# Optimization experiments

Measured on AMD Instinct MI355X. Metric: run time of the kernel, lower is better.

## Reference

```python
import jax, jax.numpy as jnp
import numpy as np

N = 50000      # nodes
E = 800000     # edges
F_IN = 128     # input features
H = 8          # heads
F = 16         # features per head
NEG_SLOPE = 0.2


def setup_inputs() -> dict:
    key = jax.random.key(0)
    k_x, k_ei, k_w, k_as, k_ad = jax.random.split(key, 5)
    x = jax.random.normal(k_x, (N, F_IN), dtype=jnp.float32)
    edge_index = jax.random.randint(k_ei, (2, E), 0, N, dtype=jnp.int64)
    # learned params (PyG GATConv: lin weight [H*F, F_in] no bias; att_src/att_dst [H, F]; out bias [H*F])
    glorot = lambda k, shp: jax.random.uniform(k, shp, jnp.float32, -1.0, 1.0) * np.sqrt(6.0 / (shp[-1] + shp[-2]))
    W = glorot(k_w, (H * F, F_IN))
    att_src = glorot(k_as, (H, F))
    att_dst = glorot(k_ad, (H, F))
    bias = jnp.zeros((H * F,), dtype=jnp.float32)  # bias_init = zeros_
    return {"x": x, "W": W, "att_src": att_src, "att_dst": att_dst, "bias": bias, "edge_index": edge_index}


def reference(x, W, att_src, att_dst, bias, edge_index):
    # linear projection, split heads: [N, H, F]
    h = (x @ W.T).reshape(N, H, F)
    # per-node attention logits: [N, H]
    a_src = jnp.einsum('nhf,hf->nh', h, att_src)
    a_dst = jnp.einsum('nhf,hf->nh', h, att_dst)
    src, dst = edge_index[0], edge_index[1]
    # edge scores + LeakyReLU: [E, H]
    e = a_src[src] + a_dst[dst]
    e = jnp.where(e >= 0, e, NEG_SLOPE * e)
    # segment softmax over incoming edges of each dst node
    m = jax.ops.segment_max(e, dst, num_segments=N)          # [N, H]
    ex = jnp.exp(e - m[dst])                                  # [E, H]
    denom = jax.ops.segment_sum(ex, dst, num_segments=N)     # [N, H]
    alpha = ex / (denom[dst] + 1e-16)                         # [E, H]
    # weighted scatter-aggregate of source features
    msg = alpha[:, :, None] * h[src]                          # [E, H, F]
    out = jax.ops.segment_sum(msg, dst, num_segments=N)      # [N, H, F]
    return out.reshape(N, H * F) + bias
```

## Files before the change

kernel.cpp:

```cpp
#include <hip/hip_runtime.h>

#define NEG_SLOPE 0.2f
#define HEADS 8
#define FEAT 16
#define HF 128
#define FIN 128
#define BROWS 64
#define PITCH 136
#define BSHIFT 7
#define BNODES 128
#define MAXBUCK 512
#define EPT 16
#define SCAP 64
#define CAP 4096

typedef __bf16 bf16x8 __attribute__((ext_vector_type(8)));
typedef float  f32x4  __attribute__((ext_vector_type(4)));

__device__ __forceinline__ bool detect_i64(const int* ei) {
    return (ei[1] | ei[3] | ei[5] | ei[7]) == 0;
}
__device__ __forceinline__ int load_idx(const int* ei, long long pos, bool is64) {
    return is64 ? ei[2 * pos] : ei[pos];
}

__device__ __forceinline__ float bf2f(unsigned u) { return __uint_as_float(u << 16); }

__device__ __forceinline__ unsigned short f2bf(float f) {
    unsigned u = __float_as_uint(f);
    unsigned r = u + 0x7fffu + ((u >> 16) & 1u);
    return (unsigned short)(r >> 16);
}

__global__ __launch_bounds__(256) void proj_binsort_kernel(
    const float* __restrict__ x, const float* __restrict__ W,
    const float* __restrict__ att_src, const float* __restrict__ att_dst,
    unsigned short* __restrict__ hb, float* __restrict__ a_src,
    float* __restrict__ a_dst,
    const int* __restrict__ ei, unsigned* __restrict__ ebuf,
    int* __restrict__ cnt2, int N, int E, int nb, int nsb, int PB)
{
    __shared__ __align__(16) char smem[(BROWS + FIN) * PITCH * 2];
    const int t = threadIdx.x;

    if (blockIdx.x >= PB) {
        int* lh = (int*)smem;
        const int blk = blockIdx.x - PB;
        const bool is64 = detect_i64(ei);
        const int e0 = blk * (EPT * 256);

        for (int b = t; b < nb; b += 256) lh[b] = 0;
        __syncthreads();

#pragma unroll
        for (int i = 0; i < EPT; ++i) {
            const int e = e0 + i * 256 + t;
            if (e < E) {
                const unsigned s = (unsigned)load_idx(ei, e, is64);
                const unsigned d = (unsigned)load_idx(ei, (long long)E + e, is64);
                const unsigned pk = s | (d << 16);
                const int bkt = d >> BSHIFT;
                const int ofs = atomicAdd(&lh[bkt], 1);
                if (ofs < SCAP)
                    ebuf[((size_t)bkt * nsb + blk) * SCAP + ofs] = pk;
            }
        }
        __syncthreads();
        for (int b = t; b < nb; b += 256)
            cnt2[blk * MAXBUCK + b] = min(lh[b], SCAP);
        return;
    }

    unsigned short* xs  = (unsigned short*)smem;
    unsigned short* wsl = xs + BROWS * PITCH;
    const int n0 = blockIdx.x * BROWS;

#pragma unroll
    for (int i = 0; i < 8; ++i) {
        const int f4 = i * 256 + t;
        const int r = f4 >> 5, c4 = f4 & 31;
        const int rr = (n0 + r < N) ? (n0 + r) : (N - 1);
        const float4 v = ((const float4*)(x + (size_t)rr * FIN))[c4];
        unsigned short* p = &xs[r * PITCH + c4 * 4];
        p[0] = f2bf(v.x); p[1] = f2bf(v.y); p[2] = f2bf(v.z); p[3] = f2bf(v.w);
    }
#pragma unroll
    for (int i = 0; i < 16; ++i) {
        const int f4 = i * 256 + t;
        const int r = f4 >> 5, c4 = f4 & 31;
        const float4 v = ((const float4*)(W + (size_t)r * FIN))[c4];
        unsigned short* p = &wsl[r * PITCH + c4 * 4];
        p[0] = f2bf(v.x); p[1] = f2bf(v.y); p[2] = f2bf(v.z); p[3] = f2bf(v.w);
    }
    __syncthreads();

    const int w = t >> 6, lane = t & 63;
    const int lrow = lane & 15;
    const int lk = lane >> 4;
    const int r0 = w * 16;

    f32x4 acc[8];
#pragma unroll
    for (int i = 0; i < 8; ++i) { f32x4 z = {0.f, 0.f, 0.f, 0.f}; acc[i] = z; }

#pragma unroll
    for (int ks = 0; ks < 4; ++ks) {
        const int kb = ks * 32 + lk * 8;
        const bf16x8 af = *(const bf16x8*)&xs[(r0 + lrow) * PITCH + kb];
#pragma unroll
        for (int tt = 0; tt < 8; ++tt) {
            const bf16x8 bf = *(const bf16x8*)&wsl[(tt * 16 + lrow) * PITCH + kb];
            acc[tt] = __builtin_amdgcn_mfma_f32_16x16x32_bf16(af, bf, acc[tt], 0, 0, 0);
        }
    }
    __syncthreads();

#pragma unroll
    for (int tt = 0; tt < 8; ++tt) {
#pragma unroll
        for (int rg = 0; rg < 4; ++rg) {
            const int row = r0 + lk * 4 + rg;
            const int col = tt * 16 + lrow;
            xs[row * PITCH + col] = f2bf(acc[tt][rg]);
        }
    }
    __syncthreads();

#pragma unroll
    for (int i = 0; i < 8; ++i) {
        const int u4 = i * 256 + t;
        const int r = u4 >> 5, c4 = u4 & 31;
        if (n0 + r < N) {
            const unsigned short* p = &xs[r * PITCH + c4 * 4];
            ushort4 v; v.x = p[0]; v.y = p[1]; v.z = p[2]; v.w = p[3];
            ((ushort4*)hb)[(size_t)(n0 + r) * (HF / 4) + c4] = v;
        }
    }
#pragma unroll
    for (int i = 0; i < 2; ++i) {
        const int p = i * 256 + t;
        const int r = p >> 3, hd = p & 7;
        if (n0 + r < N) {
            float s = 0.f, d = 0.f;
#pragma unroll
            for (int j = 0; j < FEAT; ++j) {
                const float hv = bf2f(xs[r * PITCH + hd * FEAT + j]);
                s = fmaf(hv, att_src[hd * FEAT + j], s);
                d = fmaf(hv, att_dst[hd * FEAT + j], d);
            }
            a_src[(size_t)(n0 + r) * HEADS + hd] = s;
            a_dst[(size_t)(n0 + r) * HEADS + hd] = d;
        }
    }
}

__global__ __launch_bounds__(256) void bucket_csr(
    const unsigned* __restrict__ ebuf, const int* __restrict__ cnt2,
    int* __restrict__ row_start, int* __restrict__ csr_src,
    int* __restrict__ btot, int N, int nsb)
{
    __shared__ int scnt[256], soff[256];
    __shared__ unsigned ubuf[CAP];
    __shared__ int cnts[BNODES], sc[BNODES], cur[BNODES];
    const int b = blockIdx.x;
    const int t = threadIdx.x;

    const int v = (t < nsb) ? cnt2[t * MAXBUCK + b] : 0;
    scnt[t] = v;
    soff[t] = v;
    __syncthreads();
#pragma unroll
    for (int off = 1; off < 256; off <<= 1) {
        const int y = (t >= off) ? soff[t - off] : 0;
        __syncthreads();
        soff[t] += y;
        __syncthreads();
    }
    const int cntb = min(soff[255], CAP);
    const int myoff = soff[t] - v;
    __syncthreads();

    if (t < nsb && v > 0) {
        const unsigned* sp = ebuf + ((size_t)b * nsb + t) * SCAP;
        for (int j = 0; j < v; ++j) {
            const int o = myoff + j;
            if (o < CAP) ubuf[o] = sp[j];
        }
    }
    if (t < BNODES) cnts[t] = 0;
    __syncthreads();

    for (int j = t; j < cntb; j += 256)
        atomicAdd(&cnts[(ubuf[j] >> 16) & (BNODES - 1)], 1);
    __syncthreads();
    if (t < BNODES) sc[t] = cnts[t];
    __syncthreads();
#pragma unroll
    for (int off = 1; off < BNODES; off <<= 1) {
        const int y = (t < BNODES && t >= off) ? sc[t - off] : 0;
        __syncthreads();
        if (t < BNODES) sc[t] += y;
        __syncthreads();
    }
    if (t < BNODES) {
        const int excl = sc[t] - cnts[t];
        const int node = b * BNODES + t;
        if (node < N) row_start[node] = b * CAP + excl;
        cur[t] = excl;
    }
    if (t == 0) btot[b] = cntb;
    __syncthreads();
    for (int j = t; j < cntb; j += 256) {
        const unsigned p = ubuf[j];
        const int dl = (p >> 16) & (BNODES - 1);
        const int ofs = atomicAdd(&cur[dl], 1);
        csr_src[(size_t)b * CAP + ofs] = (int)(p & 0xffffu);
    }
}

__global__ __launch_bounds__(64) void agg_kernel(
    const int* __restrict__ csr_src, const int* __restrict__ row_start,
    const int* __restrict__ btot, const float* __restrict__ a_src,
    const float* __restrict__ a_dst, const unsigned short* __restrict__ hb,
    const float* __restrict__ bias, float* __restrict__ out, int N)
{
    const int d = blockIdx.x;
    const int t = threadIdx.x;
    const int hd = t >> 3;
    const int b = d >> BSHIFT, dl = d & (BNODES - 1);
    const int beg = row_start[d];
    const int end = (dl == BNODES - 1 || d == N - 1)
                  ? (b * CAP + btot[b]) : row_start[d + 1];
    const float adh = a_dst[d * HEADS + hd];

    float acc0 = 0.f, acc1 = 0.f, den = 0.f;
    for (int c = beg; c < end; c += 64) {
        const int m = min(64, end - c);
        const int sreg = (t < m) ? csr_src[c + t] : 0;
        int j = 0;
        for (; j + 8 <= m; j += 8) {
            int s[8]; unsigned p[8]; float w[8];
#pragma unroll
            for (int k = 0; k < 8; ++k) s[k] = __shfl(sreg, j + k, 64);
#pragma unroll
            for (int k = 0; k < 8; ++k)
                p[k] = *(const unsigned*)(hb + (size_t)s[k] * HF + 2 * t);
#pragma unroll
            for (int k = 0; k < 8; ++k) {
                float v = a_src[s[k] * HEADS + hd] + adh;
                v = v >= 0.f ? v : NEG_SLOPE * v;
                w[k] = __expf(v);
            }
#pragma unroll
            for (int k = 0; k < 8; ++k) {
                acc0 = fmaf(w[k], bf2f(p[k] & 0xffffu), acc0);
                acc1 = fmaf(w[k], bf2f(p[k] >> 16),     acc1);
                den += w[k];
            }
        }
        for (; j + 4 <= m; j += 4) {
            int s[4]; unsigned p[4]; float w[4];
#pragma unroll
            for (int k = 0; k < 4; ++k) s[k] = __shfl(sreg, j + k, 64);
#pragma unroll
            for (int k = 0; k < 4; ++k)
                p[k] = *(const unsigned*)(hb + (size_t)s[k] * HF + 2 * t);
#pragma unroll
            for (int k = 0; k < 4; ++k) {
                float v = a_src[s[k] * HEADS + hd] + adh;
                v = v >= 0.f ? v : NEG_SLOPE * v;
                w[k] = __expf(v);
            }
#pragma unroll
            for (int k = 0; k < 4; ++k) {
                acc0 = fmaf(w[k], bf2f(p[k] & 0xffffu), acc0);
                acc1 = fmaf(w[k], bf2f(p[k] >> 16),     acc1);
                den += w[k];
            }
        }
        for (; j < m; ++j) {
            const int s = __shfl(sreg, j, 64);
            const unsigned p = *(const unsigned*)(hb + (size_t)s * HF + 2 * t);
            float v = a_src[s * HEADS + hd] + adh;
            v = v >= 0.f ? v : NEG_SLOPE * v;
            const float w = __expf(v);
            acc0 = fmaf(w, bf2f(p & 0xffffu), acc0);
            acc1 = fmaf(w, bf2f(p >> 16), acc1);
            den += w;
        }
    }
    const float inv = 1.f / (den + 1e-16f);
    const float2 b2 = ((const float2*)bias)[t];
    float2 o2;
    o2.x = fmaf(acc0, inv, b2.x);
    o2.y = fmaf(acc1, inv, b2.y);
    ((float2*)out)[(size_t)d * (HF / 2) + t] = o2;
}

extern "C" void kernel_launch(void* const* d_in, const int* in_sizes, int n_in,
                              void* d_out, int out_size, void* d_ws, size_t ws_size,
                              hipStream_t stream)
{
    const float* x       = (const float*)d_in[0];
    const float* W       = (const float*)d_in[1];
    const float* att_src = (const float*)d_in[2];
    const float* att_dst = (const float*)d_in[3];
    const float* bias    = (const float*)d_in[4];
    const int*   ei      = (const int*)d_in[5];
    float* out = (float*)d_out;

    const int N = in_sizes[0] / FIN;
    const int E = in_sizes[5] / 2;
    const int NBUCK = (N + BNODES - 1) >> BSHIFT;
    const int NSB = (E + EPT * 256 - 1) / (EPT * 256);
    const int PB = (N + BROWS - 1) / BROWS;

    char* ws = (char*)d_ws;
    unsigned short* hb = (unsigned short*)ws; ws += (size_t)N * HF * 2;
    unsigned* ebuf = (unsigned*)ws; ws += (size_t)NBUCK * NSB * SCAP * 4;
    int* csr_src   = (int*)ws;  ws += (size_t)NBUCK * CAP * 4;
    int* cnt2      = (int*)ws;  ws += (size_t)NSB * MAXBUCK * sizeof(int);
    float* a_src  = (float*)ws; ws += (size_t)N * HEADS * sizeof(float);
    float* a_dst  = (float*)ws; ws += (size_t)N * HEADS * sizeof(float);
    int* row_start = (int*)ws;  ws += ((size_t)N + 1) * sizeof(int);
    int* btot      = (int*)ws;

    hipLaunchKernelGGL(proj_binsort_kernel, dim3(PB + NSB), dim3(256), 0, stream,
                       x, W, att_src, att_dst, hb, a_src, a_dst,
                       ei, ebuf, cnt2, N, E, NBUCK, NSB, PB);
    hipLaunchKernelGGL(bucket_csr, dim3(NBUCK), dim3(256), 0, stream,
                       ebuf, cnt2, row_start, csr_src, btot, N, NSB);
    hipLaunchKernelGGL(agg_kernel, dim3(N), dim3(64), 0, stream,
                       csr_src, row_start, btot, a_src, a_dst, hb, bias, out, N);
}
```

Before: 154.4 us.

## Fuse bucket CSR build with aggregation, sorting edges in shared memory

Merges the bucket_csr and agg_kernel launches into one kernel. Each block sorts its bucket's edges by destination in LDS, then four waves aggregate the bucket's nodes straight from the sorted LDS array. This drops the global csr_src/row_start/btot round trip and one launch. Buckets shrink from 128 to 64 nodes, with matching capacity constants. The risk is fewer blocks (NBUCK about 782) with serial per-wave node loops, which lowers parallelism and load balance compared with one block per node.

```diff
diff --git a/kernel.cpp b/kernel.cpp
--- a/kernel.cpp
+++ b/kernel.cpp
@@ -7,12 +7,12 @@
 #define FIN 128
 #define BROWS 64
 #define PITCH 136
-#define BSHIFT 7
-#define BNODES 128
-#define MAXBUCK 512
+#define BSHIFT 6
+#define BNODES 64
+#define MAXBUCK 1024
 #define EPT 16
-#define SCAP 64
-#define CAP 4096
+#define SCAP 32
+#define CAP 2048
 
 typedef __bf16 bf16x8 __attribute__((ext_vector_type(8)));
 typedef float  f32x4  __attribute__((ext_vector_type(4)));
@@ -154,19 +154,20 @@
     }
 }
 
-__global__ __launch_bounds__(256) void bucket_csr(
+__global__ __launch_bounds__(256) void bucket_agg(
     const unsigned* __restrict__ ebuf, const int* __restrict__ cnt2,
-    int* __restrict__ row_start, int* __restrict__ csr_src,
-    int* __restrict__ btot, int N, int nsb)
+    const float* __restrict__ a_src, const float* __restrict__ a_dst,
+    const unsigned short* __restrict__ hb, const float* __restrict__ bias,
+    float* __restrict__ out, int N, int nsb)
 {
-    __shared__ int scnt[256], soff[256];
+    __shared__ int soff[256];
     __shared__ unsigned ubuf[CAP];
+    __shared__ unsigned srt[CAP];
     __shared__ int cnts[BNODES], sc[BNODES], cur[BNODES];
     const int b = blockIdx.x;
     const int t = threadIdx.x;
 
     const int v = (t < nsb) ? cnt2[t * MAXBUCK + b] : 0;
-    scnt[t] = v;
     soff[t] = v;
     __syncthreads();
 #pragma unroll
@@ -202,99 +203,87 @@
         if (t < BNODES) sc[t] += y;
         __syncthreads();
     }
-    if (t < BNODES) {
-        const int excl = sc[t] - cnts[t];
-        const int node = b * BNODES + t;
-        if (node < N) row_start[node] = b * CAP + excl;
-        cur[t] = excl;
-    }
-    if (t == 0) btot[b] = cntb;
+    if (t < BNODES) cur[t] = sc[t] - cnts[t];
     __syncthreads();
     for (int j = t; j < cntb; j += 256) {
         const unsigned p = ubuf[j];
         const int dl = (p >> 16) & (BNODES - 1);
         const int ofs = atomicAdd(&cur[dl], 1);
-        csr_src[(size_t)b * CAP + ofs] = (int)(p & 0xffffu);
-    }
-}
-
-__global__ __launch_bounds__(64) void agg_kernel(
-    const int* __restrict__ csr_src, const int* __restrict__ row_start,
-    const int* __restrict__ btot, const float* __restrict__ a_src,
-    const float* __restrict__ a_dst, const unsigned short* __restrict__ hb,
-    const float* __restrict__ bias, float* __restrict__ out, int N)
-{
-    const int d = blockIdx.x;
-    const int t = threadIdx.x;
-    const int hd = t >> 3;
-    const int b = d >> BSHIFT, dl = d & (BNODES - 1);
-    const int beg = row_start[d];
-    const int end = (dl == BNODES - 1 || d == N - 1)
-                  ? (b * CAP + btot[b]) : row_start[d + 1];
-    const float adh = a_dst[d * HEADS + hd];
-
-    float acc0 = 0.f, acc1 = 0.f, den = 0.f;
-    for (int c = beg; c < end; c += 64) {
-        const int m = min(64, end - c);
-        const int sreg = (t < m) ? csr_src[c + t] : 0;
-        int j = 0;
-        for (; j + 8 <= m; j += 8) {
-            int s[8]; unsigned p[8]; float w[8];
-#pragma unroll
-            for (int k = 0; k < 8; ++k) s[k] = __shfl(sreg, j + k, 64);
+        srt[ofs] = p & 0xffffu;
+    }
+    __syncthreads();
+
+    const int w = t >> 6, lane = t & 63;
+    const int hd = lane >> 3;
+    const float2 b2 = ((const float2*)bias)[lane];
+
+#pragma unroll 1
+    for (int i = 0; i < BNODES / 4; ++i) {
+        const int dl = w * (BNODES / 4) + i;
+        const int d = b * BNODES + dl;
+        if (d >= N) break;
+        const int end = sc[dl];
+        const int beg = end - cnts[dl];
+        const float adh = a_dst[d * HEADS + hd];
+
+        float acc0 = 0.f, acc1 = 0.f, den = 0.f;
+        int j = beg;
+        for (; j + 8 <= end; j += 8) {
+            int s[8]; unsigned p[8]; float wg[8];
+#pragma unroll
+            for (int k = 0; k < 8; ++k) s[k] = (int)srt[j + k];
 #pragma unroll
             for (int k = 0; k < 8; ++k)
-                p[k] = *(const unsigned*)(hb + (size_t)s[k] * HF + 2 * t);
+                p[k] = *(const unsigned*)(hb + (size_t)s[k] * HF + 2 * lane);
 #pragma unroll
             for (int k = 0; k < 8; ++k) {
-                float v = a_src[s[k] * HEADS + hd] + adh;
-                v = v >= 0.f ? v : NEG_SLOPE * v;
-                w[k] = __expf(v);
+                float vv = a_src[s[k] * HEADS + hd] + adh;
+                vv = vv >= 0.f ? vv : NEG_SLOPE * vv;
+                wg[k] = __expf(vv);
             }
 #pragma unroll
             for (int k = 0; k < 8; ++k) {
-                acc0 = fmaf(w[k], bf2f(p[k] & 0xffffu), acc0);
-                acc1 = fmaf(w[k], bf2f(p[k] >> 16),     acc1);
-                den += w[k];
-            }
-        }
-        for (; j + 4 <= m; j += 4) {
-            int s[4]; unsigned p[4]; float w[4];
-#pragma unroll
-            for (int k = 0; k < 4; ++k) s[k] = __shfl(sreg, j + k, 64);
+                acc0 = fmaf(wg[k], bf2f(p[k] & 0xffffu), acc0);
+                acc1 = fmaf(wg[k], bf2f(p[k] >> 16),     acc1);
+                den += wg[k];
+            }
+        }
+        for (; j + 4 <= end; j += 4) {
+            int s[4]; unsigned p[4]; float wg[4];
+#pragma unroll
+            for (int k = 0; k < 4; ++k) s[k] = (int)srt[j + k];
 #pragma unroll
             for (int k = 0; k < 4; ++k)
-                p[k] = *(const unsigned*)(hb + (size_t)s[k] * HF + 2 * t);
+                p[k] = *(const unsigned*)(hb + (size_t)s[k] * HF + 2 * lane);
 #pragma unroll
             for (int k = 0; k < 4; ++k) {
-                float v = a_src[s[k] * HEADS + hd] + adh;
-                v = v >= 0.f ? v : NEG_SLOPE * v;
-                w[k] = __expf(v);
+                float vv = a_src[s[k] * HEADS + hd] + adh;
+                vv = vv >= 0.f ? vv : NEG_SLOPE * vv;
+                wg[k] = __expf(vv);
             }
 #pragma unroll
             for (int k = 0; k < 4; ++k) {
-                acc0 = fmaf(w[k], bf2f(p[k] & 0xffffu), acc0);
-                acc1 = fmaf(w[k], bf2f(p[k] >> 16),     acc1);
-                den += w[k];
-            }
-        }
-        for (; j < m; ++j) {
-            const int s = __shfl(sreg, j, 64);
-            const unsigned p = *(const unsigned*)(hb + (size_t)s * HF + 2 * t);
-            float v = a_src[s * HEADS + hd] + adh;
-            v = v >= 0.f ? v : NEG_SLOPE * v;
-            const float w = __expf(v);
-            acc0 = fmaf(w, bf2f(p & 0xffffu), acc0);
-            acc1 = fmaf(w, bf2f(p >> 16), acc1);
-            den += w;
-        }
-    }
-    const float inv = 1.f / (den + 1e-16f);
-    const float2 b2 = ((const float2*)bias)[t];
-    float2 o2;
-    o2.x = fmaf(acc0, inv, b2.x);
-    o2.y = fmaf(acc1, inv, b2.y);
-    ((float2*)out)[(size_t)d * (HF / 2) + t] = o2;
+                acc0 = fmaf(wg[k], bf2f(p[k] & 0xffffu), acc0);
+                acc1 = fmaf(wg[k], bf2f(p[k] >> 16),     acc1);
+                den += wg[k];
+            }
+        }
+        for (; j < end; ++j) {
+            const int s = (int)srt[j];
+            const unsigned p = *(const unsigned*)(hb + (size_t)s * HF + 2 * lane);
+            float vv = a_src[s * HEADS + hd] + adh;
+            vv = vv >= 0.f ? vv : NEG_SLOPE * vv;
+            const float wg = __expf(vv);
+            acc0 = fmaf(wg, bf2f(p & 0xffffu), acc0);
+            acc1 = fmaf(wg, bf2f(p >> 16), acc1);
+            den += wg;
+        }
+        const float inv = 1.f / (den + 1e-16f);
+        float2 o2;
+        o2.x = fmaf(acc0, inv, b2.x);
+        o2.y = fmaf(acc1, inv, b2.y);
+        ((float2*)out)[(size_t)d * (HF / 2) + lane] = o2;
+    }
 }
 
 extern "C" void kernel_launch(void* const* d_in, const int* in_sizes, int n_in,
@@ -318,18 +307,13 @@
     char* ws = (char*)d_ws;
     unsigned short* hb = (unsigned short*)ws; ws += (size_t)N * HF * 2;
     unsigned* ebuf = (unsigned*)ws; ws += (size_t)NBUCK * NSB * SCAP * 4;
-    int* csr_src   = (int*)ws;  ws += (size_t)NBUCK * CAP * 4;
     int* cnt2      = (int*)ws;  ws += (size_t)NSB * MAXBUCK * sizeof(int);
     float* a_src  = (float*)ws; ws += (size_t)N * HEADS * sizeof(float);
     float* a_dst  = (float*)ws; ws += (size_t)N * HEADS * sizeof(float);
-    int* row_start = (int*)ws;  ws += ((size_t)N + 1) * sizeof(int);
-    int* btot      = (int*)ws;
 
     hipLaunchKernelGGL(proj_binsort_kernel, dim3(PB + NSB), dim3(256), 0, stream,
                        x, W, att_src, att_dst, hb, a_src, a_dst,
                        ei, ebuf, cnt2, N, E, NBUCK, NSB, PB);
-    hipLaunchKernelGGL(bucket_csr, dim3(NBUCK), dim3(256), 0, stream,
-                       ebuf, cnt2, row_start, csr_src, btot, N, NSB);
-    hipLaunchKernelGGL(agg_kernel, dim3(N), dim3(64), 0, stream,
-                       csr_src, row_start, btot, a_src, a_dst, hb, bias, out, N);
-}
+    hipLaunchKernelGGL(bucket_agg, dim3(NBUCK), dim3(256), 0, stream,
+                       ebuf, cnt2, a_src, a_dst, hb, bias, out, N, NSB);
+}
```

After: 161.5 us. +4.6%, slower.
